# Kernel tuning notes

Measured on AMD Instinct MI355X. Metric: run time of the kernel, lower is better.

## Reference

```python
import jax, jax.numpy as jnp
import numpy as np

E = 1024; H = 16; D = E // H; L = 16
B = 4; TB = 1024; TW = 512
SCALE = D ** -0.5


def _rel_matrix(S):
    r = jnp.arange(S)
    return jnp.clip(r[None, :] - r[:, None], -L, L) + L  # [S,S] ints in [0, 2L]


def _heads(x):
    # [T, b, E] -> [b*H, T, D]
    T, b, _ = x.shape
    return x.reshape(T, b * H, D).transpose(1, 0, 2)


def _rel_logits(q, table, S):
    # Shaw-style relative-key logits without materializing [S,S,D] embeddings:
    # q: [n, S, D], table: [2L+1, D] -> [n, S, S]
    mat = _rel_matrix(S)                          # [S, S]
    all_r = jnp.einsum('ntd,rd->ntr', q, table)   # [n, S, 2L+1]
    return jnp.take_along_axis(all_r, mat[None, :, :], axis=2)


def setup_inputs() -> dict:
    key = jax.random.key(0)
    ks = jax.random.split(key, 10)
    s = 0.02
    w = lambda k, shape: jax.random.normal(k, shape, jnp.float32) * s
    return {
        'query_bpe': jax.random.normal(ks[0], (TB, B, E), jnp.float32),
        'query_word': jax.random.normal(ks[1], (TW, B, E), jnp.float32),
        'mapping': jax.random.uniform(ks[2], (B, TB, TW), jnp.float32),
        'Wq_bpe': w(ks[3], (E, E)), 'bq_bpe': jnp.zeros((E,), jnp.float32),
        'Wk_bpe': w(ks[4], (E, E)), 'bk_bpe': jnp.zeros((E,), jnp.float32),
        'Wq_word': w(ks[5], (E, E)), 'bq_word': jnp.zeros((E,), jnp.float32),
        'Wk_word': w(ks[6], (E, E)), 'bk_word': jnp.zeros((E,), jnp.float32),
        'Wv': w(ks[7], (E, E)), 'bv': jnp.zeros((E,), jnp.float32),
        'Wo': w(ks[8], (E, E)), 'bo': jnp.zeros((E,), jnp.float32),
        'rel_keys_bpe': w(ks[9], (2 * L + 1, D)),
    }


def reference(query_bpe, query_word, mapping, Wq_bpe, bq_bpe, Wk_bpe, bk_bpe,
              Wq_word, bq_word, Wk_word, bk_word, Wv, bv, Wo, bo, rel_keys_bpe):
    b = query_bpe.shape[1]
    q_bpe = _heads((query_bpe @ Wq_bpe.T + bq_bpe) * SCALE)    # [bH, TB, D]
    k_bpe = _heads(query_bpe @ Wk_bpe.T + bk_bpe)
    q_word = _heads((query_word @ Wq_word.T + bq_word) * SCALE)  # [bH, TW, D]
    k_word = _heads(query_word @ Wk_word.T + bk_word)
    v = _heads(query_bpe @ Wv.T + bv)
    # content + relative-position logits for both streams
    # (k_only path in source looks up relative_position_keys_bpe for BOTH streams)
    attn_bpe = q_bpe @ k_bpe.transpose(0, 2, 1) + _rel_logits(q_bpe, rel_keys_bpe, TB)
    attn_word = q_word @ k_word.transpose(0, 2, 1) + _rel_logits(q_word, rel_keys_bpe, TW)
    aw = attn_word.reshape(b, H, TW, TW)
    # fuse word-level scores into BPE positions via alignment mapping: M A M^T
    fused = jnp.einsum('bqw,bhws->bhqs', mapping, aw)
    fused = jnp.einsum('bhqs,bks->bhqk', fused, mapping)
    attn = attn_bpe.reshape(b, H, TB, TB) + fused
    probs = jax.nn.softmax(attn, axis=-1)
    out = jnp.einsum('bhqk,bhkd->bhqd', probs, v.reshape(b, H, TB, D))
    out = out.transpose(2, 0, 1, 3).reshape(TB, b, E)  # back to [T, B, E]
    return out @ Wo.T + bo
```

## Files before the change

### kernel.cpp

```cpp
#include <hip/hip_runtime.h>


#define DEV __device__ __forceinline__
#define GAS(x) ((const __attribute__((address_space(1))) unsigned*)(x))
#define LAS(x) ((__attribute__((address_space(3))) unsigned*)(x))

typedef unsigned short u16;
typedef __attribute__((ext_vector_type(8))) short short8;
typedef __attribute__((ext_vector_type(8))) _Float16 half8;
typedef __attribute__((ext_vector_type(4))) float floatx4;

DEV float bf2f(u16 u) { union { unsigned u; float f; } v; v.u = ((unsigned)u) << 16; return v.f; }
DEV u16 f2bf(float f) {
  union { float f; unsigned u; } v; v.f = f;
  unsigned r = v.u + 0x7FFFu + ((v.u >> 16) & 1u);
  return (u16)(r >> 16);
}
DEV u16 f2h_bits(float f) { union { _Float16 h; u16 u; } v; v.h = (_Float16)f; return v.u; }

DEV void stage_u16(const u16* g, int ld, u16* lds, int tid) {
#pragma unroll
  for (int p = 0; p < 2; ++p) {
    int o = (p * 256 + tid) * 16;
    int r = o >> 6, c = (o >> 4) & 3, sc = c ^ ((r >> 1) & 3);
    __builtin_amdgcn_global_load_lds(GAS(g + (size_t)r * ld + sc * 8),
                                     LAS((char*)lds + o), 16, 0, 0);
  }
}

DEV void stage_u16_half(const u16* g, int ld, u16* lds, int tid, int p) {
  int o = (p * 256 + tid) * 16;
  int r = o >> 6, c = (o >> 4) & 3, sc = c ^ ((r >> 1) & 3);
  __builtin_amdgcn_global_load_lds(GAS(g + (size_t)(r - p * 64) * ld + sc * 8),
                                   LAS((char*)lds + o), 16, 0, 0);
}

DEV void stage_f32_bf(const float* g, int ld, u16* lds, int tid) {
#pragma unroll
  for (int p = 0; p < 2; ++p) {
    int o = (p * 256 + tid) * 16;
    int r = o >> 6, c = (o >> 4) & 3, sc = c ^ ((r >> 1) & 3);
    const float* src = g + (size_t)r * ld + sc * 8;
    union { short8 s; u16 u[8]; } oh;
#pragma unroll
    for (int j = 0; j < 8; ++j) oh.u[j] = f2bf(src[j]);
    *(short8*)((char*)lds + o) = oh.s;
  }
}

DEV void stage_f32_split(const float* g, int ld, u16* ldsh, u16* ldsl, int tid) {
#pragma unroll
  for (int p = 0; p < 2; ++p) {
    int o = (p * 256 + tid) * 16;
    int r = o >> 6, c = (o >> 4) & 3, sc = c ^ ((r >> 1) & 3);
    const float* src = g + (size_t)r * ld + sc * 8;
    union { short8 s; u16 u[8]; } oh, ol;
#pragma unroll
    for (int j = 0; j < 8; ++j) {
      float f = src[j];
      u16 h = f2bf(f);
      oh.u[j] = h;
      ol.u[j] = f2bf(f - bf2f(h));
    }
    *(short8*)((char*)ldsh + o) = oh.s;
    *(short8*)((char*)ldsl + o) = ol.s;
  }
}

DEV short8 frag_ld(const u16* lds, int row, int quad) {
  int c = quad ^ ((row >> 1) & 3);
  return *(const short8*)(lds + row * 32 + c * 8);
}

DEV void mma_bf16(const u16* As, const u16* Bs, int wr, int wc, int m, int quad, floatx4 acc[4][4]) {
  short8 af[4], bf[4];
#pragma unroll
  for (int t = 0; t < 4; ++t) af[t] = frag_ld(As, wr * 64 + t * 16 + m, quad);
#pragma unroll
  for (int t = 0; t < 4; ++t) bf[t] = frag_ld(Bs, wc * 64 + t * 16 + m, quad);
#pragma unroll
  for (int rt = 0; rt < 4; ++rt)
#pragma unroll
    for (int ct = 0; ct < 4; ++ct)
      acc[rt][ct] = __builtin_amdgcn_mfma_f32_16x16x32_bf16(af[rt], bf[ct], acc[rt][ct], 0, 0, 0);
}

DEV void mma_f16(const u16* As, const u16* Bs, int wr, int wc, int m, int quad, floatx4 acc[4][4]) {
  union { short8 s; half8 h; } af[4], bf[4];
#pragma unroll
  for (int t = 0; t < 4; ++t) af[t].s = frag_ld(As, wr * 64 + t * 16 + m, quad);
#pragma unroll
  for (int t = 0; t < 4; ++t) bf[t].s = frag_ld(Bs, wc * 64 + t * 16 + m, quad);
#pragma unroll
  for (int rt = 0; rt < 4; ++rt)
#pragma unroll
    for (int ct = 0; ct < 4; ++ct)
      acc[rt][ct] = __builtin_amdgcn_mfma_f32_16x16x32_f16(af[rt].h, bf[ct].h, acc[rt][ct], 0, 0, 0);
}

DEV void mma_split(const u16* AsH, const u16* AsL, const u16* BsH, const u16* BsL,
                   int wr, int wc, int m, int quad, floatx4 acc[4][4]) {
  short8 ah[4], al[4], bh[4], bl[4];
#pragma unroll
  for (int t = 0; t < 4; ++t) {
    ah[t] = frag_ld(AsH, wr * 64 + t * 16 + m, quad);
    al[t] = frag_ld(AsL, wr * 64 + t * 16 + m, quad);
    bh[t] = frag_ld(BsH, wc * 64 + t * 16 + m, quad);
    bl[t] = frag_ld(BsL, wc * 64 + t * 16 + m, quad);
  }
#pragma unroll
  for (int rt = 0; rt < 4; ++rt)
#pragma unroll
    for (int ct = 0; ct < 4; ++ct) {
      acc[rt][ct] = __builtin_amdgcn_mfma_f32_16x16x32_bf16(ah[rt], bh[ct], acc[rt][ct], 0, 0, 0);
      acc[rt][ct] = __builtin_amdgcn_mfma_f32_16x16x32_bf16(ah[rt], bl[ct], acc[rt][ct], 0, 0, 0);
      acc[rt][ct] = __builtin_amdgcn_mfma_f32_16x16x32_bf16(al[rt], bh[ct], acc[rt][ct], 0, 0, 0);
    }
}

DEV void acc_zero(floatx4 acc[4][4]) {
  floatx4 z = {0.f, 0.f, 0.f, 0.f};
#pragma unroll
  for (int i = 0; i < 4; ++i)
#pragma unroll
    for (int j = 0; j < 4; ++j) acc[i][j] = z;
}

struct CvtB { const float* src[5]; u16* dst[5]; int n8[5]; };
__global__ __launch_bounds__(256) void cvt_bf_kernel(CvtB a) {
  int z = blockIdx.z;
  int i = blockIdx.x * 256 + threadIdx.x;
  if (i >= a.n8[z]) return;
  const float* s = a.src[z] + (size_t)i * 8;
  union { short8 v; u16 u[8]; } o;
#pragma unroll
  for (int j = 0; j < 8; ++j) o.u[j] = f2bf(s[j]);
  *(short8*)(a.dst[z] + (size_t)i * 8) = o.v;
}

struct CvtS { const float* src[3]; u16* dh[3]; u16* dl[3]; int n8[3]; };
__global__ __launch_bounds__(256) void cvt_split_kernel(CvtS a) {
  int z = blockIdx.z;
  int i = blockIdx.x * 256 + threadIdx.x;
  if (i >= a.n8[z]) return;
  const float* s = a.src[z] + (size_t)i * 8;
  union { short8 v; u16 u[8]; } oh, ol;
#pragma unroll
  for (int j = 0; j < 8; ++j) {
    float f = s[j];
    u16 h = f2bf(f);
    oh.u[j] = h;
    ol.u[j] = f2bf(f - bf2f(h));
  }
  *(short8*)(a.dh[z] + (size_t)i * 8) = oh.v;
  *(short8*)(a.dl[z] + (size_t)i * 8) = ol.v;
}

struct PAll {
  const float* Xf[5]; const float* Wf[5];
  const u16* Xh[5]; const u16* Xl[5]; const u16* Wh[5]; const u16* Wl[5];
  const float* bias[5]; float scale[5];
  u16* dh[5]; u16* dl[5]; int T[5]; int md[5]; int prep;
};

__global__ __launch_bounds__(256) void proj_all_kernel(PAll a) {
  const int z = blockIdx.z;
  const int T = a.T[z];
  if ((int)blockIdx.y >= (T >> 5)) return;
  __shared__ __align__(16) u16 LB[8][4096];
  const int tid = threadIdx.x;
  const int lane = tid & 63, wv = tid >> 6, wr = wv >> 1, wc = wv & 1;
  const int m = lane & 15, quad = lane >> 4;
  const int md = a.md[z], prep = a.prep;
  const int bx = blockIdx.x, by = blockIdx.y;
  const size_t arow = (size_t)by * 128 * 1024;
  const size_t brow = (size_t)bx * 128 * 1024;
  floatx4 acc[4][4];
  acc_zero(acc);
  if (prep) {
    if (md == 2) {
      stage_u16(a.Xh[z] + arow, 1024, LB[0], tid);
      stage_u16(a.Wh[z] + brow, 1024, LB[2], tid);
      stage_u16(a.Xl[z] + arow, 1024, LB[4], tid);
      stage_u16(a.Wl[z] + brow, 1024, LB[6], tid);
    } else {
      stage_u16(a.Xh[z] + arow, 1024, LB[0], tid);
      stage_u16(a.Wh[z] + brow, 1024, LB[2], tid);
    }
    __syncthreads();
    for (int k0 = 0; k0 < 1024; k0 += 32) {
      int cur = (k0 >> 5) & 1, nx = cur ^ 1;
      if (k0 + 32 < 1024) {
        if (md == 2) {
          stage_u16(a.Xh[z] + arow + k0 + 32, 1024, LB[nx], tid);
          stage_u16(a.Wh[z] + brow + k0 + 32, 1024, LB[2 + nx], tid);
          stage_u16(a.Xl[z] + arow + k0 + 32, 1024, LB[4 + nx], tid);
          stage_u16(a.Wl[z] + brow + k0 + 32, 1024, LB[6 + nx], tid);
        } else {
          stage_u16(a.Xh[z] + arow + k0 + 32, 1024, LB[nx], tid);
          stage_u16(a.Wh[z] + brow + k0 + 32, 1024, LB[2 + nx], tid);
        }
      }
      if (md == 2) mma_split(LB[cur], LB[4 + cur], LB[2 + cur], LB[6 + cur], wr, wc, m, quad, acc);
      else         mma_bf16(LB[cur], LB[2 + cur], wr, wc, m, quad, acc);
      __syncthreads();
    }
  } else {
    for (int k0 = 0; k0 < 1024; k0 += 32) {
      __syncthreads();
      if (md == 2) {
        stage_f32_split(a.Xf[z] + arow + k0, 1024, LB[0], LB[4], tid);
        stage_f32_split(a.Wf[z] + brow + k0, 1024, LB[2], LB[6], tid);
      } else {
        stage_f32_bf(a.Xf[z] + arow + k0, 1024, LB[0], tid);
        stage_f32_bf(a.Wf[z] + brow + k0, 1024, LB[2], tid);
      }
      __syncthreads();
      if (md == 2) mma_split(LB[0], LB[4], LB[2], LB[6], wr, wc, m, quad, acc);
      else         mma_bf16(LB[0], LB[2], wr, wc, m, quad, acc);
    }
    __syncthreads();
  }
  const float scale = a.scale[z];
  const float* bias = a.bias[z];
  u16* dh = a.dh[z];
  u16* dl = a.dl[z];
  const int row0l = wr * 64 + quad * 4;
  const int col0l = wc * 64 + m;
  if (md == 0) {
#pragma unroll
    for (int rt = 0; rt < 4; ++rt)
#pragma unroll
      for (int ct = 0; ct < 4; ++ct) {
        int col = bx * 128 + col0l + ct * 16;
        float bi = bias[col];
        int h = col >> 6, d = col & 63;
#pragma unroll
        for (int rg = 0; rg < 4; ++rg) {
          int row = by * 128 + row0l + rt * 16 + rg;
          int t = row >> 2, bb = row & 3, n = bb * 16 + h;
          float val = (acc[rt][ct][rg] + bi) * scale;
          dh[((size_t)n * T + t) * 64 + d] = f2bf(val);
        }
      }
  } else if (md == 1) {
    u16* TB = (u16*)LB;
    __syncthreads();
#pragma unroll
    for (int rt = 0; rt < 4; ++rt)
#pragma unroll
      for (int ct = 0; ct < 4; ++ct) {
        int cl = col0l + ct * 16;
        float bi = bias[bx * 128 + cl];
#pragma unroll
        for (int rg = 0; rg < 4; ++rg) {
          int rl = row0l + rt * 16 + rg;
          TB[(size_t)cl * 130 + rl] = f2bf((acc[rt][ct][rg] + bi) * scale);
        }
      }
    __syncthreads();
    for (int task = tid; task < 512; task += 256) {
      int c = task & 127, bb = task >> 7;
      int colg = bx * 128 + c, h = colg >> 6, d = colg & 63;
      size_t base = (((size_t)(bb * 16 + h)) * 64 + d) * 1024 + (size_t)by * 32;
#pragma unroll
      for (int g = 0; g < 4; ++g) {
        union { short8 v; u16 u[8]; } o;
#pragma unroll
        for (int j = 0; j < 8; ++j) o.u[j] = TB[(size_t)c * 130 + bb + 4 * (g * 8 + j)];
        *(short8*)(dh + base + g * 8) = o.v;
      }
    }
  } else {
    u16* TBh = (u16*)LB;
    u16* TBl = TBh + 64 * 130;
    for (int pass = 0; pass < 2; ++pass) {
      __syncthreads();
      if (wc == pass) {
#pragma unroll
        for (int rt = 0; rt < 4; ++rt)
#pragma unroll
          for (int ct = 0; ct < 4; ++ct) {
            int cl = ct * 16 + m;
            float bi = bias[bx * 128 + pass * 64 + cl];
#pragma unroll
            for (int rg = 0; rg < 4; ++rg) {
              int rl = row0l + rt * 16 + rg;
              float val = (acc[rt][ct][rg] + bi) * scale;
              u16 hh = f2bf(val);
              TBh[(size_t)cl * 130 + rl] = hh;
              TBl[(size_t)cl * 130 + rl] = f2bf(val - bf2f(hh));
            }
          }
      }
      __syncthreads();
      int c2 = tid & 63, bb = tid >> 6;
      int colg = bx * 128 + pass * 64 + c2, h = colg >> 6, d = colg & 63;
      size_t base = (((size_t)(bb * 16 + h)) * 64 + d) * 512 + (size_t)by * 32;
#pragma unroll
      for (int g = 0; g < 4; ++g) {
        union { short8 v; u16 u[8]; } oh, ol;
#pragma unroll
        for (int j = 0; j < 8; ++j) {
          oh.u[j] = TBh[(size_t)c2 * 130 + bb + 4 * (g * 8 + j)];
          ol.u[j] = TBl[(size_t)c2 * 130 + bb + 4 * (g * 8 + j)];
        }
        *(short8*)(dh + base + g * 8) = oh.v;
        *(short8*)(dl + base + g * 8) = ol.v;
      }
    }
  }
}

__global__ __launch_bounds__(256) void msplit_kernel(const float* __restrict__ M,
                                                     u16* __restrict__ Mh, u16* __restrict__ Ml,
                                                     u16* __restrict__ Mf) {
  int i = blockIdx.x * 256 + threadIdx.x;
  float f = M[i];
  u16 h = f2bf(f);
  Mh[i] = h;
  Ml[i] = f2bf(f - bf2f(h));
  Mf[i] = f2h_bits(f);
}

__global__ __launch_bounds__(256) void rel_bpe_kernel(const u16* __restrict__ q,
                                                      const float* __restrict__ relk,
                                                      float* __restrict__ R) {
  int nt = blockIdx.x * 256 + threadIdx.x;
  float qv[64];
#pragma unroll
  for (int c = 0; c < 8; ++c) {
    union { short8 s; u16 u[8]; } uh; uh.s = *(const short8*)(q + (size_t)nt * 64 + c * 8);
#pragma unroll
    for (int j = 0; j < 8; ++j) qv[c * 8 + j] = bf2f(uh.u[j]);
  }
  for (int r = 0; r < 33; ++r) {
    const float* krow = relk + r * 64;
    float s = 0.f;
#pragma unroll
    for (int d = 0; d < 64; ++d) s += qv[d] * krow[d];
    R[(size_t)nt * 33 + r] = s;
  }
}

__global__ __launch_bounds__(256) void rel_word_kernel(const u16* __restrict__ qh, const u16* __restrict__ ql,
                                                       const float* __restrict__ relk,
                                                       float* __restrict__ R) {
  int nt = blockIdx.x * 256 + threadIdx.x;
  int n = nt >> 9, w = nt & 511;
  float qv[64];
#pragma unroll
  for (int d = 0; d < 64; ++d) {
    size_t idx = ((size_t)n * 64 + d) * 512 + w;
    qv[d] = bf2f(qh[idx]) + bf2f(ql[idx]);
  }
  for (int r = 0; r < 33; ++r) {
    const float* krow = relk + r * 64;
    float s = 0.f;
#pragma unroll
    for (int d = 0; d < 64; ++d) s += qv[d] * krow[d];
    R[(size_t)nt * 33 + r] = s;
  }
}

__global__ __launch_bounds__(256) void relmat64_kernel(const float* __restrict__ Rw,
                                                       u16* __restrict__ RT, int n0) {
  int i = blockIdx.x * 256 + threadIdx.x;
  int w8 = i & 7, s = (i >> 3) & 31, t = (i >> 8) & 15, nl = i >> 12;
  int n = n0 + nl;
  int w0 = (t == 0) ? 0 : (t == 15 ? 448 : 32 * t - 16);
  int sg = t * 32 + s;
  const float* R = Rw + (size_t)n * 512 * 33;
  union { short8 v; u16 u[8]; } o;
#pragma unroll
  for (int j = 0; j < 8; ++j) {
    int w = w0 + w8 * 8 + j;
    int d = sg - w; d = d < -16 ? -16 : (d > 16 ? 16 : d);
    o.u[j] = f2h_bits(R[(size_t)w * 33 + d + 16]);
  }
  *(short8*)(RT + (size_t)i * 8) = o.v;
}

__global__ __launch_bounds__(256) void prefix16_kernel(const u16* __restrict__ Mf,
                                                       const float* __restrict__ Rw,
                                                       float* __restrict__ PS, int n0) {
  const int nl = blockIdx.y, n = n0 + nl, b = n >> 4;
  const int q = blockIdx.x * 256 + threadIdx.x;
  const u16* mrow = Mf + ((size_t)b * 1024 + q) * 512;
  const float* R = Rw + (size_t)n * 512 * 33;
  float* ps = PS + ((size_t)nl * 1024 + q) * 66;
  float blkA[32], blkB[32];
#pragma unroll
  for (int t = 0; t < 32; ++t) {
    float a = 0.f, bb = 0.f;
#pragma unroll
    for (int c = 0; c < 2; ++c) {
      union { short8 s; _Float16 h[8]; } u;
      u.s = *(const short8*)(mrow + t * 16 + c * 8);
#pragma unroll
      for (int j = 0; j < 8; ++j) {
        int w = t * 16 + c * 8 + j;
        float mv = (float)u.h[j];
        a += mv * R[(size_t)w * 33 + 32];
        bb += mv * R[(size_t)w * 33];
      }
    }
    blkA[t] = a; blkB[t] = bb;
  }
  float run = 0.f;
#pragma unroll
  for (int i = 0; i < 33; ++i) { ps[i] = run; if (i < 32) run += blkA[i]; }
  float tot = 0.f;
#pragma unroll
  for (int i = 0; i < 32; ++i) tot += blkB[i];
  run = tot;
#pragma unroll
  for (int i = 0; i < 33; ++i) { ps[33 + i] = run; if (i < 32) run -= blkB[i]; }
}

__global__ __launch_bounds__(256) void stage1band_kernel(const u16* __restrict__ Mf,
                                                         const u16* __restrict__ RT,
                                                         const float* __restrict__ PS,
                                                         u16* __restrict__ C1r, int n0) {
  __shared__ __align__(16) u16 As[4096], Bs[1024];
  const int tid = threadIdx.x, t = blockIdx.x, nl = blockIdx.z, n = n0 + nl, b = n >> 4;
  const int lane = tid & 63, wv = tid >> 6;
  const int m = lane & 15, quad = lane >> 4;
  const int w0 = (t == 0) ? 0 : (t == 15 ? 448 : 32 * t - 16);
  const size_t ma = ((size_t)b * 1024 + blockIdx.y * 128) * 512 + w0;
  const u16* rt = RT + ((size_t)nl * 16 + t) * 2048;
  floatx4 acc[2][2];
  floatx4 z = {0.f, 0.f, 0.f, 0.f};
  acc[0][0] = z; acc[0][1] = z; acc[1][0] = z; acc[1][1] = z;
#pragma unroll
  for (int k0 = 0; k0 < 64; k0 += 32) {
    __syncthreads();
    stage_u16(Mf + ma + k0, 512, As, tid);
    if (tid < 128) {
      int o = tid * 16;
      int r = o >> 6, c = (o >> 4) & 3, sc = c ^ ((r >> 1) & 3);
      __builtin_amdgcn_global_load_lds(GAS(rt + k0 + (size_t)r * 64 + sc * 8),
                                       LAS((char*)Bs + o), 16, 0, 0);
    }
    __syncthreads();
    union { short8 s; half8 h; } af[2], bf[2];
#pragma unroll
    for (int i = 0; i < 2; ++i) af[i].s = frag_ld(As, wv * 32 + i * 16 + m, quad);
#pragma unroll
    for (int i = 0; i < 2; ++i) bf[i].s = frag_ld(Bs, i * 16 + m, quad);
#pragma unroll
    for (int i = 0; i < 2; ++i)
#pragma unroll
      for (int j = 0; j < 2; ++j)
        acc[i][j] = __builtin_amdgcn_mfma_f32_16x16x32_f16(af[i].h, bf[j].h, acc[i][j], 0, 0, 0);
  }
  const int ia = w0 >> 4, ib = (w0 + 64) >> 4;
  const float* ps = PS + ((size_t)nl * 1024 + blockIdx.y * 128) * 66;
#pragma unroll
  for (int i = 0; i < 2; ++i)
#pragma unroll
    for (int rg = 0; rg < 4; ++rg) {
      int row = wv * 32 + i * 16 + quad * 4 + rg;
      float ab = ps[(size_t)row * 66 + ia] + ps[(size_t)row * 66 + 33 + ib];
      int q = blockIdx.y * 128 + row;
#pragma unroll
      for (int j = 0; j < 2; ++j) {
        int s = t * 32 + j * 16 + m;
        C1r[((size_t)nl * 1024 + q) * 512 + s] = f2h_bits(acc[i][j][rg] + ab);
      }
    }
}

__global__ __launch_bounds__(256) void mqk_kernel(const u16* __restrict__ Mh, const u16* __restrict__ Ml,
                                                  const u16* __restrict__ qwTh, const u16* __restrict__ qwTl,
                                                  const u16* __restrict__ kwTh, const u16* __restrict__ kwTl,
                                                  u16* __restrict__ MQh, u16* __restrict__ MQl,
                                                  u16* __restrict__ MKh, u16* __restrict__ MKl, int n0) {
  __shared__ __align__(16) u16 AsH[4096], AsL[4096], BsH[4096], BsL[4096];
  const int tid = threadIdx.x, nl = blockIdx.y, n = n0 + nl, b = n >> 4;
  const int lane = tid & 63, wv = tid >> 6, wr = wv >> 1, wc = wv & 1;
  const int m = lane & 15, quad = lane >> 4;
  const size_t ma = ((size_t)b * 1024 + blockIdx.x * 128) * 512;
  const u16* Qh = qwTh + (size_t)n * 32768;
  const u16* Ql = qwTl + (size_t)n * 32768;
  const u16* Kh = kwTh + (size_t)n * 32768;
  const u16* Kl = kwTl + (size_t)n * 32768;
  floatx4 acc[4][4];
  acc_zero(acc);
  for (int k0 = 0; k0 < 512; k0 += 32) {
    __syncthreads();
    stage_u16(Mh + ma + k0, 512, AsH, tid);
    stage_u16(Ml + ma + k0, 512, AsL, tid);
    stage_u16_half(Qh + k0, 512, BsH, tid, 0);
    stage_u16_half(Kh + k0, 512, BsH, tid, 1);
    stage_u16_half(Ql + k0, 512, BsL, tid, 0);
    stage_u16_half(Kl + k0, 512, BsL, tid, 1);
    __syncthreads();
    mma_split(AsH, AsL, BsH, BsL, wr, wc, m, quad, acc);
  }
  u16* dsth = wc ? MKh : MQh;
  u16* dstl = wc ? MKl : MQl;
  const int row0 = blockIdx.x * 128 + wr * 64 + quad * 4;
#pragma unroll
  for (int rt = 0; rt < 4; ++rt)
#pragma unroll
    for (int ct = 0; ct < 4; ++ct) {
      int d = (ct * 16 + m) & 63;
#pragma unroll
      for (int rg = 0; rg < 4; ++rg) {
        int row = row0 + rt * 16 + rg;
        size_t idx = ((size_t)nl * 1024 + row) * 64 + d;
        float val = acc[rt][ct][rg];
        u16 hh = f2bf(val);
        dsth[idx] = hh;
        dstl[idx] = f2bf(val - bf2f(hh));
      }
    }
}

__global__ __launch_bounds__(256) void logits_kernel(const u16* __restrict__ qb, const u16* __restrict__ kb,
                                                     const u16* __restrict__ MQh, const u16* __restrict__ MQl,
                                                     const u16* __restrict__ MKh, const u16* __restrict__ MKl,
                                                     const u16* __restrict__ C1r, const u16* __restrict__ Mf,
                                                     const float* __restrict__ Rb, u16* __restrict__ L,
                                                     int n0) {
  __shared__ __align__(16) u16 LB[8][4096];
  const int tid = threadIdx.x, nl = blockIdx.z, n = n0 + nl, b = n >> 4;
  const int bq = blockIdx.x, bk = blockIdx.y;
  const int lane = tid & 63, wv = tid >> 6, wr = wv >> 1, wc = wv & 1;
  const int m = lane & 15, quad = lane >> 4;
  const size_t qa = ((size_t)n * 1024 + bq * 128) * 64;
  const size_t ka = ((size_t)n * 1024 + bk * 128) * 64;
  const size_t mqa = ((size_t)nl * 1024 + bq * 128) * 64;
  const size_t mka = ((size_t)nl * 1024 + bk * 128) * 64;
  const size_t ca = ((size_t)nl * 1024 + bq * 128) * 512;
  const size_t ma = ((size_t)b * 1024 + bk * 128) * 512;
  floatx4 acc[4][4];
  acc_zero(acc);
  stage_u16(qb + qa, 64, LB[0], tid);
  stage_u16(kb + ka, 64, LB[2], tid);
  __syncthreads();
  stage_u16(qb + qa + 32, 64, LB[1], tid);
  stage_u16(kb + ka + 32, 64, LB[3], tid);
  mma_bf16(LB[0], LB[2], wr, wc, m, quad, acc);
  __syncthreads();
  mma_bf16(LB[1], LB[3], wr, wc, m, quad, acc);
  __syncthreads();
  stage_u16(MQh + mqa,      64, LB[0], tid);
  stage_u16(MQh + mqa + 32, 64, LB[1], tid);
  stage_u16(MKh + mka,      64, LB[2], tid);
  stage_u16(MKh + mka + 32, 64, LB[3], tid);
  stage_u16(MQl + mqa,      64, LB[4], tid);
  stage_u16(MQl + mqa + 32, 64, LB[5], tid);
  stage_u16(MKl + mka,      64, LB[6], tid);
  stage_u16(MKl + mka + 32, 64, LB[7], tid);
  __syncthreads();
  mma_split(LB[0], LB[4], LB[2], LB[6], wr, wc, m, quad, acc);
  mma_split(LB[1], LB[5], LB[3], LB[7], wr, wc, m, quad, acc);
  __syncthreads();
  stage_u16(C1r + ca, 512, LB[0], tid);
  stage_u16(Mf + ma, 512, LB[2], tid);
  __syncthreads();
  for (int k0 = 0; k0 < 512; k0 += 32) {
    int cur = (k0 >> 5) & 1;
    if (k0 + 32 < 512) {
      stage_u16(C1r + ca + k0 + 32, 512, LB[cur ^ 1], tid);
      stage_u16(Mf + ma + k0 + 32, 512, LB[2 + (cur ^ 1)], tid);
    }
    mma_f16(LB[cur], LB[2 + cur], wr, wc, m, quad, acc);
    __syncthreads();
  }
  const int q0 = bq * 128 + wr * 64 + quad * 4;
  const int k0c = bk * 128 + wc * 64 + m;
#pragma unroll
  for (int rt = 0; rt < 4; ++rt)
#pragma unroll
    for (int ct = 0; ct < 4; ++ct) {
      int kc = k0c + ct * 16;
#pragma unroll
      for (int rg = 0; rg < 4; ++rg) {
        int q = q0 + rt * 16 + rg;
        int id = kc - q; id = id < -16 ? -16 : (id > 16 ? 16 : id); id += 16;
        float val = acc[rt][ct][rg] + Rb[((size_t)n * 1024 + q) * 33 + id];
        L[((size_t)nl * 1024 + q) * 1024 + kc] = f2h_bits(val);
      }
    }
}

__global__ __launch_bounds__(256) void softmax_pv_kernel(const u16* __restrict__ L,
                                                         const u16* __restrict__ VT,
                                                         u16* __restrict__ AO, int n0) {
  __shared__ __align__(16) u16 Vs[2][4][2048];
  const int tid = threadIdx.x, lane = tid & 63, wv = tid >> 6;
  const int m = lane & 15, quad = lane >> 4;
  const int nl = blockIdx.y, n = n0 + nl, qt = blockIdx.x;
  const int qrow = qt * 64 + wv * 16 + m;
  const u16* Lrow = L + ((size_t)nl * 1024 + qrow) * 1024;
  const u16* Vbase = VT + (size_t)n * 64 * 1024;
  float mi = -1e30f, li = 0.f;
  floatx4 O[4];
  floatx4 z = {0.f, 0.f, 0.f, 0.f};
#pragma unroll
  for (int dt = 0; dt < 4; ++dt) O[dt] = z;

  auto stageV = [&](int kt, int buf) {
#pragma unroll
    for (int ct = 0; ct < 4; ++ct) {
      int o = tid * 16;
      int r = o >> 6, c = (o >> 4) & 3, sc = c ^ ((r >> 1) & 3);
      __builtin_amdgcn_global_load_lds(GAS(Vbase + (size_t)r * 1024 + kt * 128 + ct * 32 + sc * 8),
                                       LAS((char*)Vs[buf][ct] + o), 16, 0, 0);
    }
  };
  stageV(0, 0);
  __syncthreads();

  for (int kt = 0; kt < 8; ++kt) {
    int cur = kt & 1;
    if (kt + 1 < 8) stageV(kt + 1, cur ^ 1);

    float vals[4][8];
#pragma unroll
    for (int ct = 0; ct < 4; ++ct) {
      union { short8 s; _Float16 h[8]; } u;
      u.s = *(const short8*)(Lrow + kt * 128 + ct * 32 + quad * 8);
#pragma unroll
      for (int j = 0; j < 8; ++j) vals[ct][j] = (float)u.h[j];
    }
    float tmax = vals[0][0];
#pragma unroll
    for (int ct = 0; ct < 4; ++ct)
#pragma unroll
      for (int j = 0; j < 8; ++j) tmax = fmaxf(tmax, vals[ct][j]);
    tmax = fmaxf(tmax, __shfl_xor(tmax, 16));
    tmax = fmaxf(tmax, __shfl_xor(tmax, 32));
    float mnew = fmaxf(mi, tmax);
    float alpha = __expf(mi - mnew);
    float pv[4][8];
    float tsum = 0.f;
#pragma unroll
    for (int ct = 0; ct < 4; ++ct)
#pragma unroll
      for (int j = 0; j < 8; ++j) { pv[ct][j] = __expf(vals[ct][j] - mnew); tsum += pv[ct][j]; }
    tsum += __shfl_xor(tsum, 16);
    tsum += __shfl_xor(tsum, 32);
    li = li * alpha + tsum;
    mi = mnew;

    float ar[4];
#pragma unroll
    for (int rg = 0; rg < 4; ++rg) ar[rg] = __shfl(alpha, quad * 4 + rg);
#pragma unroll
    for (int dt = 0; dt < 4; ++dt)
#pragma unroll
      for (int rg = 0; rg < 4; ++rg) O[dt][rg] *= ar[rg];

    short8 pf[4];
#pragma unroll
    for (int ct = 0; ct < 4; ++ct) {
      union { short8 s; u16 us[8]; } up;
#pragma unroll
      for (int j = 0; j < 8; ++j) up.us[j] = f2bf(pv[ct][j]);
      pf[ct] = up.s;
    }
#pragma unroll
    for (int ct = 0; ct < 4; ++ct)
#pragma unroll
      for (int dt = 0; dt < 4; ++dt) {
        short8 vf = frag_ld(Vs[cur][ct], dt * 16 + m, quad);
        O[dt] = __builtin_amdgcn_mfma_f32_16x16x32_bf16(pf[ct], vf, O[dt], 0, 0, 0);
      }
    __syncthreads();
  }

  float linv = 1.f / li;
  float lr[4];
#pragma unroll
  for (int rg = 0; rg < 4; ++rg) lr[rg] = __shfl(linv, quad * 4 + rg);
  const int b = n >> 4, h = n & 15;
#pragma unroll
  for (int dt = 0; dt < 4; ++dt)
#pragma unroll
    for (int rg = 0; rg < 4; ++rg) {
      int q = qt * 64 + wv * 16 + quad * 4 + rg;
      float ov = O[dt][rg] * lr[rg];
      AO[((size_t)q * 4 + b) * 1024 + h * 64 + dt * 16 + m] = f2bf(ov);
    }
}

__global__ __launch_bounds__(256) void outproj_kernel(const u16* __restrict__ AO, const float* __restrict__ Wo,
                                                      const u16* __restrict__ Wob, int prep,
                                                      const float* __restrict__ bo, float* __restrict__ out) {
  __shared__ __align__(16) u16 LB[4][4096];
  const int tid = threadIdx.x;
  const int lane = tid & 63, wv = tid >> 6, wr = wv >> 1, wc = wv & 1;
  const int m = lane & 15, quad = lane >> 4;
  const u16* A = AO + (size_t)blockIdx.y * 128 * 1024;
  const size_t brow = (size_t)blockIdx.x * 128 * 1024;
  floatx4 acc[4][4];
  acc_zero(acc);
  if (prep) {
    stage_u16(A, 1024, LB[0], tid);
    stage_u16(Wob + brow, 1024, LB[2], tid);
    __syncthreads();
    for (int k0 = 0; k0 < 1024; k0 += 32) {
      int cur = (k0 >> 5) & 1;
      if (k0 + 32 < 1024) {
        stage_u16(A + k0 + 32, 1024, LB[cur ^ 1], tid);
        stage_u16(Wob + brow + k0 + 32, 1024, LB[2 + (cur ^ 1)], tid);
      }
      mma_bf16(LB[cur], LB[2 + cur], wr, wc, m, quad, acc);
      __syncthreads();
    }
  } else {
    for (int k0 = 0; k0 < 1024; k0 += 32) {
      __syncthreads();
      stage_u16(A + k0, 1024, LB[0], tid);
      stage_f32_bf(Wo + brow + k0, 1024, LB[2], tid);
      __syncthreads();
      mma_bf16(LB[0], LB[2], wr, wc, m, quad, acc);
    }
  }
  const int r0 = blockIdx.y * 128 + wr * 64 + quad * 4;
  const int c0 = blockIdx.x * 128 + wc * 64 + m;
#pragma unroll
  for (int rt = 0; rt < 4; ++rt)
#pragma unroll
    for (int ct = 0; ct < 4; ++ct) {
      int col = c0 + ct * 16;
      float bi = bo[col];
#pragma unroll
      for (int rg = 0; rg < 4; ++rg) {
        int row = r0 + rt * 16 + rg;
        out[(size_t)row * 1024 + col] = acc[rt][ct][rg] + bi;
      }
    }
}

extern "C" void kernel_launch(void* const* d_in, const int* in_sizes, int n_in,
                              void* d_out, int out_size, void* d_ws, size_t ws_size,
                              hipStream_t stream) {
  const float* query_bpe = (const float*)d_in[0];
  const float* query_word = (const float*)d_in[1];
  const float* mapping = (const float*)d_in[2];
  const float* Wq_bpe = (const float*)d_in[3];
  const float* bq_bpe = (const float*)d_in[4];
  const float* Wk_bpe = (const float*)d_in[5];
  const float* bk_bpe = (const float*)d_in[6];
  const float* Wq_word = (const float*)d_in[7];
  const float* bq_word = (const float*)d_in[8];
  const float* Wk_word = (const float*)d_in[9];
  const float* bk_word = (const float*)d_in[10];
  const float* Wv = (const float*)d_in[11];
  const float* bv = (const float*)d_in[12];
  const float* Wo = (const float*)d_in[13];
  const float* bo = (const float*)d_in[14];
  const float* relk = (const float*)d_in[15];

  char* ws = (char*)d_ws;
  size_t off = 0;
  u16* q_bpe = (u16*)(ws + off); off += 8388608;
  u16* k_bpe = (u16*)(ws + off); off += 8388608;
  u16* VTb   = (u16*)(ws + off); off += 8388608;
  u16* qwT_h = (u16*)(ws + off); off += 4194304;
  u16* qwT_l = (u16*)(ws + off); off += 4194304;
  u16* kwT_h = (u16*)(ws + off); off += 4194304;
  u16* kwT_l = (u16*)(ws + off); off += 4194304;
  u16* M_h   = (u16*)(ws + off); off += 4194304;
  u16* M_l   = (u16*)(ws + off); off += 4194304;
  u16* M_f   = (u16*)(ws + off); off += 4194304;
  float* R_word = (float*)(ws + off); off += 4325376;
  float* R_bpe  = (float*)(ws + off); off += 8650752;
  u16* AO    = (u16*)(ws + off); off += 8388608;
  u16* Wo_bf = (u16*)(ws + off); off += 2097152;
  const size_t fixed_end = off;

  const size_t avail = (ws_size > fixed_end) ? ws_size - fixed_end : 0;
  const int prep = avail >= 31457280 ? 1 : 0;
  const size_t per_nc = 4005888;
  int NC = 1;
  for (int c = 64; c >= 1; c >>= 1) {
    if ((size_t)c * per_nc <= avail) { NC = c; break; }
  }
  char* vb = ws + fixed_end;
  u16* RelT  = (u16*)(vb);
  float* PS  = (float*)(vb + (size_t)NC * 65536);
  u16* C1r   = (u16*)(vb + (size_t)NC * 335872);
  u16* L_c   = (u16*)(vb + (size_t)NC * 1384448);
  u16* MQh   = (u16*)(vb + (size_t)NC * 3481600);
  u16* MQl   = (u16*)(vb + (size_t)NC * 3612672);
  u16* MKh   = (u16*)(vb + (size_t)NC * 3743744);
  u16* MKl   = (u16*)(vb + (size_t)NC * 3874816);
  u16* Xb    = (u16*)(vb);
  u16* Wqb   = (u16*)(vb + 8388608);
  u16* Wkb   = (u16*)(vb + 10485760);
  u16* Wvb   = (u16*)(vb + 12582912);
  u16* Xw_h  = (u16*)(vb + 14680064);
  u16* Xw_l  = (u16*)(vb + 18874368);
  u16* Wqw_h = (u16*)(vb + 23068672);
  u16* Wqw_l = (u16*)(vb + 25165824);
  u16* Wkw_h = (u16*)(vb + 27262976);
  u16* Wkw_l = (u16*)(vb + 29360128);

  if (prep) {
    CvtB cb = {};
    cb.src[0] = query_bpe; cb.dst[0] = Xb;    cb.n8[0] = 524288;
    cb.src[1] = Wq_bpe;    cb.dst[1] = Wqb;   cb.n8[1] = 131072;
    cb.src[2] = Wk_bpe;    cb.dst[2] = Wkb;   cb.n8[2] = 131072;
    cb.src[3] = Wv;        cb.dst[3] = Wvb;   cb.n8[3] = 131072;
    cb.src[4] = Wo;        cb.dst[4] = Wo_bf; cb.n8[4] = 131072;
    cvt_bf_kernel<<<dim3(2048, 1, 5), 256, 0, stream>>>(cb);
    CvtS cs = {};
    cs.src[0] = query_word; cs.dh[0] = Xw_h;  cs.dl[0] = Xw_l;  cs.n8[0] = 262144;
    cs.src[1] = Wq_word;    cs.dh[1] = Wqw_h; cs.dl[1] = Wqw_l; cs.n8[1] = 131072;
    cs.src[2] = Wk_word;    cs.dh[2] = Wkw_h; cs.dl[2] = Wkw_l; cs.n8[2] = 131072;
    cvt_split_kernel<<<dim3(1024, 1, 3), 256, 0, stream>>>(cs);
  }

  PAll pa = {};
  pa.prep = prep;
  pa.Xf[0] = query_bpe;  pa.Wf[0] = Wq_bpe;  pa.Xh[0] = Xb;   pa.Wh[0] = Wqb;
  pa.bias[0] = bq_bpe;  pa.scale[0] = 0.125f; pa.dh[0] = q_bpe; pa.T[0] = 1024; pa.md[0] = 0;
  pa.Xf[1] = query_bpe;  pa.Wf[1] = Wk_bpe;  pa.Xh[1] = Xb;   pa.Wh[1] = Wkb;
  pa.bias[1] = bk_bpe;  pa.scale[1] = 1.0f;   pa.dh[1] = k_bpe; pa.T[1] = 1024; pa.md[1] = 0;
  pa.Xf[2] = query_bpe;  pa.Wf[2] = Wv;      pa.Xh[2] = Xb;   pa.Wh[2] = Wvb;
  pa.bias[2] = bv;      pa.scale[2] = 1.0f;   pa.dh[2] = VTb;   pa.T[2] = 1024; pa.md[2] = 1;
  pa.Xf[3] = query_word; pa.Wf[3] = Wq_word; pa.Xh[3] = Xw_h; pa.Xl[3] = Xw_l;
  pa.Wh[3] = Wqw_h; pa.Wl[3] = Wqw_l;
  pa.bias[3] = bq_word; pa.scale[3] = 0.125f; pa.dh[3] = qwT_h; pa.dl[3] = qwT_l; pa.T[3] = 512; pa.md[3] = 2;
  pa.Xf[4] = query_word; pa.Wf[4] = Wk_word; pa.Xh[4] = Xw_h; pa.Xl[4] = Xw_l;
  pa.Wh[4] = Wkw_h; pa.Wl[4] = Wkw_l;
  pa.bias[4] = bk_word; pa.scale[4] = 1.0f;   pa.dh[4] = kwT_h; pa.dl[4] = kwT_l; pa.T[4] = 512; pa.md[4] = 2;
  proj_all_kernel<<<dim3(8, 32, 5), 256, 0, stream>>>(pa);

  msplit_kernel<<<dim3(4 * 1024 * 512 / 256), 256, 0, stream>>>(mapping, M_h, M_l, M_f);

  rel_bpe_kernel<<<dim3(64 * 1024 / 256), 256, 0, stream>>>(q_bpe, relk, R_bpe);
  rel_word_kernel<<<dim3(64 * 512 / 256), 256, 0, stream>>>(qwT_h, qwT_l, relk, R_word);

  for (int n0 = 0; n0 < 64; n0 += NC) {
    relmat64_kernel<<<dim3(NC * 16), 256, 0, stream>>>(R_word, RelT, n0);
    prefix16_kernel<<<dim3(4, NC), 256, 0, stream>>>(M_f, R_word, PS, n0);
    mqk_kernel<<<dim3(8, NC), 256, 0, stream>>>(M_h, M_l, qwT_h, qwT_l, kwT_h, kwT_l,
                                                MQh, MQl, MKh, MKl, n0);
    stage1band_kernel<<<dim3(16, 8, NC), 256, 0, stream>>>(M_f, RelT, PS, C1r, n0);
    logits_kernel<<<dim3(8, 8, NC), 256, 0, stream>>>(q_bpe, k_bpe, MQh, MQl, MKh, MKl,
                                                      C1r, M_f, R_bpe, L_c, n0);
    softmax_pv_kernel<<<dim3(16, NC), 256, 0, stream>>>(L_c, VTb, AO, n0);
  }

  outproj_kernel<<<dim3(8, 32), 256, 0, stream>>>(AO, Wo, Wo_bf, prep, bo, (float*)d_out);
}
```

Baseline: 730.4 us.

## Pipeline GEMM staging with vmcnt waits, fuse relmat and prefix kernels

Rewrites the double-buffered staging loops in the projection, mqk, logits and out-projection kernels. Each loop now issues the next tile's async global-to-LDS loads, waits with an explicit s_waitcnt vmcnt on only the older loads, and uses raw barriers, so the current tile is consumed while the next is in flight. mqk gains double buffering, stage1band prefetches both k-steps up front, and the logits kernel's LDS footprint is halved. The relmat and prefix kernels are merged into one launch per chunk to cut launch overhead. The vmcnt counts are hand-coded, so correctness depends on them matching the number of loads issued per stage.

```diff
diff --git a/kernel.cpp b/kernel.cpp
--- a/kernel.cpp
+++ b/kernel.cpp
@@ -17,6 +17,16 @@
   return (u16)(r >> 16);
 }
 DEV u16 f2h_bits(float f) { union { _Float16 h; u16 u; } v; v.h = (_Float16)f; return v.u; }
+
+template <int N> DEV void vmwait() {
+  asm volatile("s_waitcnt vmcnt(%0)" ::"n"(N) : "memory");
+  __builtin_amdgcn_sched_barrier(0);
+}
+DEV void barrier_raw() {
+  asm volatile("" ::: "memory");
+  __builtin_amdgcn_s_barrier();
+  asm volatile("" ::: "memory");
+}
 
 DEV void stage_u16(const u16* g, int ld, u16* lds, int tid) {
 #pragma unroll
@@ -178,32 +188,42 @@
   floatx4 acc[4][4];
   acc_zero(acc);
   if (prep) {
+    const u16* Xh = a.Xh[z]; const u16* Xl = a.Xl[z];
+    const u16* Wh = a.Wh[z]; const u16* Wl = a.Wl[z];
     if (md == 2) {
-      stage_u16(a.Xh[z] + arow, 1024, LB[0], tid);
-      stage_u16(a.Wh[z] + brow, 1024, LB[2], tid);
-      stage_u16(a.Xl[z] + arow, 1024, LB[4], tid);
-      stage_u16(a.Wl[z] + brow, 1024, LB[6], tid);
+      stage_u16(Xh + arow, 1024, LB[0], tid);
+      stage_u16(Wh + brow, 1024, LB[1], tid);
+      stage_u16(Xl + arow, 1024, LB[2], tid);
+      stage_u16(Wl + brow, 1024, LB[3], tid);
+      for (int k0 = 0; k0 < 1024; k0 += 32) {
+        int o = ((k0 >> 5) & 1) * 4;
+        if (k0 + 32 < 1024) {
+          int no = 4 - o;
+          stage_u16(Xh + arow + k0 + 32, 1024, LB[no], tid);
+          stage_u16(Wh + brow + k0 + 32, 1024, LB[no + 1], tid);
+          stage_u16(Xl + arow + k0 + 32, 1024, LB[no + 2], tid);
+          stage_u16(Wl + brow + k0 + 32, 1024, LB[no + 3], tid);
+          vmwait<8>();
+        } else vmwait<0>();
+        barrier_raw();
+        mma_split(LB[o], LB[o + 2], LB[o + 1], LB[o + 3], wr, wc, m, quad, acc);
+        barrier_raw();
+      }
     } else {
-      stage_u16(a.Xh[z] + arow, 1024, LB[0], tid);
-      stage_u16(a.Wh[z] + brow, 1024, LB[2], tid);
-    }
-    __syncthreads();
-    for (int k0 = 0; k0 < 1024; k0 += 32) {
-      int cur = (k0 >> 5) & 1, nx = cur ^ 1;
-      if (k0 + 32 < 1024) {
-        if (md == 2) {
-          stage_u16(a.Xh[z] + arow + k0 + 32, 1024, LB[nx], tid);
-          stage_u16(a.Wh[z] + brow + k0 + 32, 1024, LB[2 + nx], tid);
-          stage_u16(a.Xl[z] + arow + k0 + 32, 1024, LB[4 + nx], tid);
-          stage_u16(a.Wl[z] + brow + k0 + 32, 1024, LB[6 + nx], tid);
-        } else {
-          stage_u16(a.Xh[z] + arow + k0 + 32, 1024, LB[nx], tid);
-          stage_u16(a.Wh[z] + brow + k0 + 32, 1024, LB[2 + nx], tid);
-        }
-      }
-      if (md == 2) mma_split(LB[cur], LB[4 + cur], LB[2 + cur], LB[6 + cur], wr, wc, m, quad, acc);
-      else         mma_bf16(LB[cur], LB[2 + cur], wr, wc, m, quad, acc);
-      __syncthreads();
+      stage_u16(Xh + arow, 1024, LB[0], tid);
+      stage_u16(Wh + brow, 1024, LB[1], tid);
+      for (int k0 = 0; k0 < 1024; k0 += 32) {
+        int o = ((k0 >> 5) & 1) * 2;
+        if (k0 + 32 < 1024) {
+          int no = 2 - o;
+          stage_u16(Xh + arow + k0 + 32, 1024, LB[no], tid);
+          stage_u16(Wh + brow + k0 + 32, 1024, LB[no + 1], tid);
+          vmwait<4>();
+        } else vmwait<0>();
+        barrier_raw();
+        mma_bf16(LB[o], LB[o + 1], wr, wc, m, quad, acc);
+        barrier_raw();
+      }
     }
   } else {
     for (int k0 = 0; k0 < 1024; k0 += 32) {
@@ -363,91 +383,94 @@
   }
 }
 
-__global__ __launch_bounds__(256) void relmat64_kernel(const float* __restrict__ Rw,
-                                                       u16* __restrict__ RT, int n0) {
-  int i = blockIdx.x * 256 + threadIdx.x;
-  int w8 = i & 7, s = (i >> 3) & 31, t = (i >> 8) & 15, nl = i >> 12;
-  int n = n0 + nl;
-  int w0 = (t == 0) ? 0 : (t == 15 ? 448 : 32 * t - 16);
-  int sg = t * 32 + s;
-  const float* R = Rw + (size_t)n * 512 * 33;
-  union { short8 v; u16 u[8]; } o;
-#pragma unroll
-  for (int j = 0; j < 8; ++j) {
-    int w = w0 + w8 * 8 + j;
-    int d = sg - w; d = d < -16 ? -16 : (d > 16 ? 16 : d);
-    o.u[j] = f2h_bits(R[(size_t)w * 33 + d + 16]);
-  }
-  *(short8*)(RT + (size_t)i * 8) = o.v;
-}
-
-__global__ __launch_bounds__(256) void prefix16_kernel(const u16* __restrict__ Mf,
-                                                       const float* __restrict__ Rw,
-                                                       float* __restrict__ PS, int n0) {
-  const int nl = blockIdx.y, n = n0 + nl, b = n >> 4;
-  const int q = blockIdx.x * 256 + threadIdx.x;
-  const u16* mrow = Mf + ((size_t)b * 1024 + q) * 512;
-  const float* R = Rw + (size_t)n * 512 * 33;
-  float* ps = PS + ((size_t)nl * 1024 + q) * 66;
-  float blkA[32], blkB[32];
-#pragma unroll
-  for (int t = 0; t < 32; ++t) {
-    float a = 0.f, bb = 0.f;
-#pragma unroll
-    for (int c = 0; c < 2; ++c) {
-      union { short8 s; _Float16 h[8]; } u;
-      u.s = *(const short8*)(mrow + t * 16 + c * 8);
-#pragma unroll
-      for (int j = 0; j < 8; ++j) {
-        int w = t * 16 + c * 8 + j;
-        float mv = (float)u.h[j];
-        a += mv * R[(size_t)w * 33 + 32];
-        bb += mv * R[(size_t)w * 33];
-      }
-    }
-    blkA[t] = a; blkB[t] = bb;
-  }
-  float run = 0.f;
-#pragma unroll
-  for (int i = 0; i < 33; ++i) { ps[i] = run; if (i < 32) run += blkA[i]; }
-  float tot = 0.f;
-#pragma unroll
-  for (int i = 0; i < 32; ++i) tot += blkB[i];
-  run = tot;
-#pragma unroll
-  for (int i = 0; i < 33; ++i) { ps[33 + i] = run; if (i < 32) run -= blkB[i]; }
+__global__ __launch_bounds__(256) void relprefix_kernel(const float* __restrict__ Rw,
+                                                        const u16* __restrict__ Mf,
+                                                        u16* __restrict__ RT,
+                                                        float* __restrict__ PS,
+                                                        int NCx, int n0) {
+  const int bx = blockIdx.x;
+  if (bx < NCx * 16) {
+    int i = bx * 256 + threadIdx.x;
+    int w8 = i & 7, s = (i >> 3) & 31, t = (i >> 8) & 15, nl = i >> 12;
+    int n = n0 + nl;
+    int w0 = (t == 0) ? 0 : (t == 15 ? 448 : 32 * t - 16);
+    int sg = t * 32 + s;
+    const float* R = Rw + (size_t)n * 512 * 33;
+    union { short8 v; u16 u[8]; } o;
+#pragma unroll
+    for (int j = 0; j < 8; ++j) {
+      int w = w0 + w8 * 8 + j;
+      int d = sg - w; d = d < -16 ? -16 : (d > 16 ? 16 : d);
+      o.u[j] = f2h_bits(R[(size_t)w * 33 + d + 16]);
+    }
+    *(short8*)(RT + (size_t)i * 8) = o.v;
+  } else {
+    const int px = bx - NCx * 16;
+    const int nl = px >> 2, n = n0 + nl, b = n >> 4;
+    const int q = (px & 3) * 256 + threadIdx.x;
+    const u16* mrow = Mf + ((size_t)b * 1024 + q) * 512;
+    const float* R = Rw + (size_t)n * 512 * 33;
+    float* ps = PS + ((size_t)nl * 1024 + q) * 66;
+    float blkA[32], blkB[32];
+#pragma unroll
+    for (int t = 0; t < 32; ++t) {
+      float a = 0.f, bb = 0.f;
+#pragma unroll
+      for (int c = 0; c < 2; ++c) {
+        union { short8 s; _Float16 h[8]; } u;
+        u.s = *(const short8*)(mrow + t * 16 + c * 8);
+#pragma unroll
+        for (int j = 0; j < 8; ++j) {
+          int w = t * 16 + c * 8 + j;
+          float mv = (float)u.h[j];
+          a += mv * R[(size_t)w * 33 + 32];
+          bb += mv * R[(size_t)w * 33];
+        }
+      }
+      blkA[t] = a; blkB[t] = bb;
+    }
+    float run = 0.f;
+#pragma unroll
+    for (int i = 0; i < 33; ++i) { ps[i] = run; if (i < 32) run += blkA[i]; }
+    float tot = 0.f;
+#pragma unroll
+    for (int i = 0; i < 32; ++i) tot += blkB[i];
+    run = tot;
+#pragma unroll
+    for (int i = 0; i < 33; ++i) { ps[33 + i] = run; if (i < 32) run -= blkB[i]; }
+  }
 }
 
 __global__ __launch_bounds__(256) void stage1band_kernel(const u16* __restrict__ Mf,
                                                          const u16* __restrict__ RT,
                                                          const float* __restrict__ PS,
                                                          u16* __restrict__ C1r, int n0) {
-  __shared__ __align__(16) u16 As[4096], Bs[1024];
+  __shared__ __align__(16) u16 As[2][4096], Bs[2][1024];
   const int tid = threadIdx.x, t = blockIdx.x, nl = blockIdx.z, n = n0 + nl, b = n >> 4;
   const int lane = tid & 63, wv = tid >> 6;
   const int m = lane & 15, quad = lane >> 4;
   const int w0 = (t == 0) ? 0 : (t == 15 ? 448 : 32 * t - 16);
   const size_t ma = ((size_t)b * 1024 + blockIdx.y * 128) * 512 + w0;
   const u16* rt = RT + ((size_t)nl * 16 + t) * 2048;
+  stage_u16(Mf + ma, 512, As[0], tid);
+  stage_u16(Mf + ma + 32, 512, As[1], tid);
+  {
+    int half = tid >> 7, tt = tid & 127, o = tt * 16;
+    int r = o >> 6, c = (o >> 4) & 3, sc = c ^ ((r >> 1) & 3);
+    __builtin_amdgcn_global_load_lds(GAS(rt + half * 32 + (size_t)r * 64 + sc * 8),
+                                     LAS((char*)Bs[half] + o), 16, 0, 0);
+  }
   floatx4 acc[2][2];
   floatx4 z = {0.f, 0.f, 0.f, 0.f};
   acc[0][0] = z; acc[0][1] = z; acc[1][0] = z; acc[1][1] = z;
-#pragma unroll
-  for (int k0 = 0; k0 < 64; k0 += 32) {
-    __syncthreads();
-    stage_u16(Mf + ma + k0, 512, As, tid);
-    if (tid < 128) {
-      int o = tid * 16;
-      int r = o >> 6, c = (o >> 4) & 3, sc = c ^ ((r >> 1) & 3);
-      __builtin_amdgcn_global_load_lds(GAS(rt + k0 + (size_t)r * 64 + sc * 8),
-                                       LAS((char*)Bs + o), 16, 0, 0);
-    }
-    __syncthreads();
+  __syncthreads();
+#pragma unroll
+  for (int ks = 0; ks < 2; ++ks) {
     union { short8 s; half8 h; } af[2], bf[2];
 #pragma unroll
-    for (int i = 0; i < 2; ++i) af[i].s = frag_ld(As, wv * 32 + i * 16 + m, quad);
-#pragma unroll
-    for (int i = 0; i < 2; ++i) bf[i].s = frag_ld(Bs, i * 16 + m, quad);
+    for (int i = 0; i < 2; ++i) af[i].s = frag_ld(As[ks], wv * 32 + i * 16 + m, quad);
+#pragma unroll
+    for (int i = 0; i < 2; ++i) bf[i].s = frag_ld(Bs[ks], i * 16 + m, quad);
 #pragma unroll
     for (int i = 0; i < 2; ++i)
 #pragma unroll
@@ -476,7 +499,7 @@
                                                   const u16* __restrict__ kwTh, const u16* __restrict__ kwTl,
                                                   u16* __restrict__ MQh, u16* __restrict__ MQl,
                                                   u16* __restrict__ MKh, u16* __restrict__ MKl, int n0) {
-  __shared__ __align__(16) u16 AsH[4096], AsL[4096], BsH[4096], BsL[4096];
+  __shared__ __align__(16) u16 LB[8][4096];
   const int tid = threadIdx.x, nl = blockIdx.y, n = n0 + nl, b = n >> 4;
   const int lane = tid & 63, wv = tid >> 6, wr = wv >> 1, wc = wv & 1;
   const int m = lane & 15, quad = lane >> 4;
@@ -487,16 +510,24 @@
   const u16* Kl = kwTl + (size_t)n * 32768;
   floatx4 acc[4][4];
   acc_zero(acc);
+  auto stage_set = [&](int o, int k) {
+    stage_u16(Mh + ma + k, 512, LB[o], tid);
+    stage_u16(Ml + ma + k, 512, LB[o + 1], tid);
+    stage_u16_half(Qh + k, 512, LB[o + 2], tid, 0);
+    stage_u16_half(Kh + k, 512, LB[o + 2], tid, 1);
+    stage_u16_half(Ql + k, 512, LB[o + 3], tid, 0);
+    stage_u16_half(Kl + k, 512, LB[o + 3], tid, 1);
+  };
+  stage_set(0, 0);
   for (int k0 = 0; k0 < 512; k0 += 32) {
-    __syncthreads();
-    stage_u16(Mh + ma + k0, 512, AsH, tid);
-    stage_u16(Ml + ma + k0, 512, AsL, tid);
-    stage_u16_half(Qh + k0, 512, BsH, tid, 0);
-    stage_u16_half(Kh + k0, 512, BsH, tid, 1);
-    stage_u16_half(Ql + k0, 512, BsL, tid, 0);
-    stage_u16_half(Kl + k0, 512, BsL, tid, 1);
-    __syncthreads();
-    mma_split(AsH, AsL, BsH, BsL, wr, wc, m, quad, acc);
+    int o = ((k0 >> 5) & 1) * 4;
+    if (k0 + 32 < 512) {
+      stage_set(4 - o, k0 + 32);
+      vmwait<8>();
+    } else vmwait<0>();
+    barrier_raw();
+    mma_split(LB[o], LB[o + 1], LB[o + 2], LB[o + 3], wr, wc, m, quad, acc);
+    barrier_raw();
   }
   u16* dsth = wc ? MKh : MQh;
   u16* dstl = wc ? MKl : MQl;
@@ -524,7 +555,7 @@
                                                      const u16* __restrict__ C1r, const u16* __restrict__ Mf,
                                                      const float* __restrict__ Rb, u16* __restrict__ L,
                                                      int n0) {
-  __shared__ __align__(16) u16 LB[8][4096];
+  __shared__ __align__(16) u16 LB[4][4096];
   const int tid = threadIdx.x, nl = blockIdx.z, n = n0 + nl, b = n >> 4;
   const int bq = blockIdx.x, bk = blockIdx.y;
   const int lane = tid & 63, wv = tid >> 6, wr = wv >> 1, wc = wv & 1;
@@ -538,37 +569,37 @@
   floatx4 acc[4][4];
   acc_zero(acc);
   stage_u16(qb + qa, 64, LB[0], tid);
-  stage_u16(kb + ka, 64, LB[2], tid);
+  stage_u16(kb + ka, 64, LB[1], tid);
   __syncthreads();
-  stage_u16(qb + qa + 32, 64, LB[1], tid);
+  stage_u16(qb + qa + 32, 64, LB[2], tid);
   stage_u16(kb + ka + 32, 64, LB[3], tid);
-  mma_bf16(LB[0], LB[2], wr, wc, m, quad, acc);
+  mma_bf16(LB[0], LB[1], wr, wc, m, quad, acc);
   __syncthreads();
-  mma_bf16(LB[1], LB[3], wr, wc, m, quad, acc);
+  mma_bf16(LB[2], LB[3], wr, wc, m, quad, acc);
   __syncthreads();
-  stage_u16(MQh + mqa,      64, LB[0], tid);
-  stage_u16(MQh + mqa + 32, 64, LB[1], tid);
-  stage_u16(MKh + mka,      64, LB[2], tid);
-  stage_u16(MKh + mka + 32, 64, LB[3], tid);
-  stage_u16(MQl + mqa,      64, LB[4], tid);
-  stage_u16(MQl + mqa + 32, 64, LB[5], tid);
-  stage_u16(MKl + mka,      64, LB[6], tid);
-  stage_u16(MKl + mka + 32, 64, LB[7], tid);
-  __syncthreads();
-  mma_split(LB[0], LB[4], LB[2], LB[6], wr, wc, m, quad, acc);
-  mma_split(LB[1], LB[5], LB[3], LB[7], wr, wc, m, quad, acc);
-  __syncthreads();
+#pragma unroll
+  for (int k0 = 0; k0 < 64; k0 += 32) {
+    stage_u16(MQh + mqa + k0, 64, LB[0], tid);
+    stage_u16(MQl + mqa + k0, 64, LB[1], tid);
+    stage_u16(MKh + mka + k0, 64, LB[2], tid);
+    stage_u16(MKl + mka + k0, 64, LB[3], tid);
+    __syncthreads();
+    mma_split(LB[0], LB[1], LB[2], LB[3], wr, wc, m, quad, acc);
+    __syncthreads();
+  }
   stage_u16(C1r + ca, 512, LB[0], tid);
-  stage_u16(Mf + ma, 512, LB[2], tid);
-  __syncthreads();
+  stage_u16(Mf + ma, 512, LB[1], tid);
   for (int k0 = 0; k0 < 512; k0 += 32) {
-    int cur = (k0 >> 5) & 1;
+    int o = ((k0 >> 5) & 1) * 2;
     if (k0 + 32 < 512) {
-      stage_u16(C1r + ca + k0 + 32, 512, LB[cur ^ 1], tid);
-      stage_u16(Mf + ma + k0 + 32, 512, LB[2 + (cur ^ 1)], tid);
-    }
-    mma_f16(LB[cur], LB[2 + cur], wr, wc, m, quad, acc);
-    __syncthreads();
+      int no = 2 - o;
+      stage_u16(C1r + ca + k0 + 32, 512, LB[no], tid);
+      stage_u16(Mf + ma + k0 + 32, 512, LB[no + 1], tid);
+      vmwait<4>();
+    } else vmwait<0>();
+    barrier_raw();
+    mma_f16(LB[o], LB[o + 1], wr, wc, m, quad, acc);
+    barrier_raw();
   }
   const int q0 = bq * 128 + wr * 64 + quad * 4;
   const int k0c = bk * 128 + wc * 64 + m;
@@ -701,16 +732,18 @@
   acc_zero(acc);
   if (prep) {
     stage_u16(A, 1024, LB[0], tid);
-    stage_u16(Wob + brow, 1024, LB[2], tid);
-    __syncthreads();
+    stage_u16(Wob + brow, 1024, LB[1], tid);
     for (int k0 = 0; k0 < 1024; k0 += 32) {
-      int cur = (k0 >> 5) & 1;
+      int o = ((k0 >> 5) & 1) * 2;
       if (k0 + 32 < 1024) {
-        stage_u16(A + k0 + 32, 1024, LB[cur ^ 1], tid);
-        stage_u16(Wob + brow + k0 + 32, 1024, LB[2 + (cur ^ 1)], tid);
-      }
-      mma_bf16(LB[cur], LB[2 + cur], wr, wc, m, quad, acc);
-      __syncthreads();
+        int no = 2 - o;
+        stage_u16(A + k0 + 32, 1024, LB[no], tid);
+        stage_u16(Wob + brow + k0 + 32, 1024, LB[no + 1], tid);
+        vmwait<4>();
+      } else vmwait<0>();
+      barrier_raw();
+      mma_bf16(LB[o], LB[o + 1], wr, wc, m, quad, acc);
+      barrier_raw();
     }
   } else {
     for (int k0 = 0; k0 < 1024; k0 += 32) {
@@ -839,8 +872,7 @@
   rel_word_kernel<<<dim3(64 * 512 / 256), 256, 0, stream>>>(qwT_h, qwT_l, relk, R_word);
 
   for (int n0 = 0; n0 < 64; n0 += NC) {
-    relmat64_kernel<<<dim3(NC * 16), 256, 0, stream>>>(R_word, RelT, n0);
-    prefix16_kernel<<<dim3(4, NC), 256, 0, stream>>>(M_f, R_word, PS, n0);
+    relprefix_kernel<<<dim3(NC * 20), 256, 0, stream>>>(R_word, M_f, RelT, PS, NC, n0);
     mqk_kernel<<<dim3(8, NC), 256, 0, stream>>>(M_h, M_l, qwT_h, qwT_l, kwT_h, kwT_l,
                                                 MQh, MQl, MKh, MKl, n0);
     stage1band_kernel<<<dim3(16, 8, NC), 256, 0, stream>>>(M_f, RelT, PS, C1r, n0);
```

Result: faster. 627.1 us (-14.1%).
